# Kernel optimization log

Hardware: AMD Instinct MI355X
Metric: run time of the kernel (lower is better)

## Reference

```python
import jax, jax.numpy as jnp
import numpy as np

NUM_SLOTS = 16
CORE_INPUT_SIZE = 256


def _perm_matrix(key):
    p = jax.random.permutation(key, NUM_SLOTS)
    return jnp.eye(NUM_SLOTS, dtype=jnp.float32)[p]


def setup_inputs() -> dict:
    key = jax.random.key(0)
    kx, k1, k2 = jax.random.split(key, 3)
    x = jax.random.normal(kx, (512, 16, 16, CORE_INPUT_SIZE), dtype=jnp.float32)
    Ppos = _perm_matrix(k1)
    Pneg = _perm_matrix(k2)
    return {"x": x, "Ppos": Ppos, "Pneg": Pneg}


def reference(x, Ppos, Pneg):
    B, O, I, C = x.shape
    # split last dim into (num_slots rows, cols)
    xr = x.reshape(B, O, I, NUM_SLOTS, C // NUM_SLOTS)
    # permutation-matrix einsum on the slots axis (a one-hot gather)
    xpos = jnp.einsum('ij,boijk->boiik'.replace('boij', 'bOIj').replace('boii', 'bOIi'), Ppos, xr) if False else jnp.einsum('ij,...jk->...ik', Ppos, xr)
    xneg = jnp.einsum('ij,...jk->...ik', Pneg, xr)
    return (xpos - xneg).reshape(B, O, I, C)
```

## Files before the change

kernel.cpp:

```cpp
#include <hip/hip_runtime.h>


#define NSLOTS 16

__global__ __launch_bounds__(256) void permute_ws_kernel(
    const float4* __restrict__ x,
    const float* __restrict__ Ppos,
    const float* __restrict__ Pneg,
    float4* __restrict__ out,
    long total_v4)
{
    __shared__ int spos[NSLOTS];
    __shared__ int sneg[NSLOTS];

    const int t = threadIdx.x;
    if (t < NSLOTS) {
        int ip = 0, in_ = 0;
        #pragma unroll
        for (int j = 0; j < NSLOTS; ++j) {
            if (Ppos[t * NSLOTS + j] > 0.5f) ip = j;
            if (Pneg[t * NSLOTS + j] > 0.5f) in_ = j;
        }
        spos[t] = ip;
        sneg[t] = in_;
    }
    __syncthreads();

    long idx = (long)blockIdx.x * blockDim.x + threadIdx.x;
    const long stride = (long)gridDim.x * blockDim.x;

    for (; idx < total_v4; idx += stride) {
        const long row_base = idx & ~63L;
        const int  v        = (int)(idx & 63);
        const int  slot     = v >> 2;
        const int  k4       = v & 3;

        const float4 a = x[row_base + ((long)spos[slot] << 2) + k4];
        const float4 b = x[row_base + ((long)sneg[slot] << 2) + k4];

        float4 r;
        r.x = a.x - b.x;
        r.y = a.y - b.y;
        r.z = a.z - b.z;
        r.w = a.w - b.w;
        out[idx] = r;
    }
}

extern "C" void kernel_launch(void* const* d_in, const int* in_sizes, int n_in,
                              void* d_out, int out_size, void* d_ws, size_t ws_size,
                              hipStream_t stream)
{
    const float4* x    = (const float4*)d_in[0];
    const float*  Ppos = (const float*)d_in[1];
    const float*  Pneg = (const float*)d_in[2];
    float4*       out  = (float4*)d_out;

    const long total_v4 = (long)out_size / 4;

    const int block = 256;
    long blocks_needed = (total_v4 + block - 1) / block;
    int grid = (int)(blocks_needed > 32768 ? 32768 : blocks_needed);

    permute_ws_kernel<<<grid, block, 0, stream>>>(x, Ppos, Pneg, out, total_v4);
}
```

Measured before the change: 224.5 us.

## Replace gathered loads with one coalesced load and wavefront shuffles

Each thread now loads its own float4 contiguously, and the permuted source values are fetched from other lanes with __shfl, replacing two gathered global loads per output. Decoding of the permutation matrices moves into a separate tiny kernel that writes indices to workspace, which removes the per-block shared-memory decode and barrier. The change relies on each 64-lane wavefront covering exactly one 256-float row and on the grid stride staying a multiple of 64. It adds eight cross-lane shuffles per element and a second kernel launch.

Result: no change. 228.6 us (+1.9%).

```diff
diff --git a/kernel.cpp b/kernel.cpp
--- a/kernel.cpp
+++ b/kernel.cpp
@@ -3,42 +3,51 @@
 
 #define NSLOTS 16
 
+__global__ void decode_perm_kernel(const float* __restrict__ Ppos,
+                                   const float* __restrict__ Pneg,
+                                   int* __restrict__ wsi)
+{
+    const int t = threadIdx.x;
+    if (t < 2 * NSLOTS) {
+        const float* P = (t < NSLOTS) ? Ppos : Pneg;
+        const int row = t & (NSLOTS - 1);
+        int idx = 0;
+        #pragma unroll
+        for (int j = 0; j < NSLOTS; ++j)
+            if (P[row * NSLOTS + j] > 0.5f) idx = j;
+        wsi[t] = idx;
+    }
+}
+
 __global__ __launch_bounds__(256) void permute_ws_kernel(
     const float4* __restrict__ x,
-    const float* __restrict__ Ppos,
-    const float* __restrict__ Pneg,
+    const int* __restrict__ wsi,
     float4* __restrict__ out,
     long total_v4)
 {
-    __shared__ int spos[NSLOTS];
-    __shared__ int sneg[NSLOTS];
+    const int lane = threadIdx.x & 63;
+    const int slot = lane >> 2;
+    const int k4   = lane & 3;
 
-    const int t = threadIdx.x;
-    if (t < NSLOTS) {
-        int ip = 0, in_ = 0;
-        #pragma unroll
-        for (int j = 0; j < NSLOTS; ++j) {
-            if (Ppos[t * NSLOTS + j] > 0.5f) ip = j;
-            if (Pneg[t * NSLOTS + j] > 0.5f) in_ = j;
-        }
-        spos[t] = ip;
-        sneg[t] = in_;
-    }
-    __syncthreads();
+    const int src_a = (wsi[slot] << 2) | k4;
+    const int src_b = (wsi[NSLOTS + slot] << 2) | k4;
 
     long idx = (long)blockIdx.x * blockDim.x + threadIdx.x;
     const long stride = (long)gridDim.x * blockDim.x;
 
     for (; idx < total_v4; idx += stride) {
-        const long row_base = idx & ~63L;
-        const int  v        = (int)(idx & 63);
-        const int  slot     = v >> 2;
-        const int  k4       = v & 3;
+        const float4 v = x[idx];
 
-        const float4 a = x[row_base + ((long)spos[slot] << 2) + k4];
-        const float4 b = x[row_base + ((long)sneg[slot] << 2) + k4];
+        float4 a, b, r;
+        a.x = __shfl(v.x, src_a, 64);
+        a.y = __shfl(v.y, src_a, 64);
+        a.z = __shfl(v.z, src_a, 64);
+        a.w = __shfl(v.w, src_a, 64);
+        b.x = __shfl(v.x, src_b, 64);
+        b.y = __shfl(v.y, src_b, 64);
+        b.z = __shfl(v.z, src_b, 64);
+        b.w = __shfl(v.w, src_b, 64);
 
-        float4 r;
         r.x = a.x - b.x;
         r.y = a.y - b.y;
         r.z = a.z - b.z;
@@ -55,12 +64,14 @@
     const float*  Ppos = (const float*)d_in[1];
     const float*  Pneg = (const float*)d_in[2];
     float4*       out  = (float4*)d_out;
+    int*          wsi  = (int*)d_ws;
 
     const long total_v4 = (long)out_size / 4;
+
+    decode_perm_kernel<<<1, 64, 0, stream>>>(Ppos, Pneg, wsi);
 
     const int block = 256;
     long blocks_needed = (total_v4 + block - 1) / block;
     int grid = (int)(blocks_needed > 32768 ? 32768 : blocks_needed);
-
-    permute_ws_kernel<<<grid, block, 0, stream>>>(x, Ppos, Pneg, out, total_v4);
+    permute_ws_kernel<<<grid, block, 0, stream>>>(x, wsi, out, total_v4);
 }
```

## Load each row once and permute slots with wavefront shuffles

Applied to the files above, without the earlier changes.

Each thread now loads its own float4 in a coalesced way and gets the permuted values from other lanes with __shfl, instead of doing two gather loads per output. Every thread decodes the permutation indices itself, which removes the shared memory and the barrier. The grid is fixed at 2048 blocks and each iteration handles two elements to keep more loads in flight. The cost is 16 cross-lane shuffles per pair of elements. The code also assumes total_v4 is a multiple of 64 and that a wavefront holds exactly one 64-float4 row.

New measurement: 236.3 us. 1.05x slower.

```diff
diff --git a/kernel.cpp b/kernel.cpp
--- a/kernel.cpp
+++ b/kernel.cpp
@@ -10,40 +10,41 @@
     float4* __restrict__ out,
     long total_v4)
 {
-    __shared__ int spos[NSLOTS];
-    __shared__ int sneg[NSLOTS];
+    const int lane = threadIdx.x & 63;
+    const int slot = lane >> 2;
+    const int k4   = lane & 3;
 
-    const int t = threadIdx.x;
-    if (t < NSLOTS) {
-        int ip = 0, in_ = 0;
-        #pragma unroll
-        for (int j = 0; j < NSLOTS; ++j) {
-            if (Ppos[t * NSLOTS + j] > 0.5f) ip = j;
-            if (Pneg[t * NSLOTS + j] > 0.5f) in_ = j;
-        }
-        spos[t] = ip;
-        sneg[t] = in_;
+    int ip = 0, in_ = 0;
+    #pragma unroll
+    for (int j = 0; j < NSLOTS; ++j) {
+        if (Ppos[slot * NSLOTS + j] > 0.5f) ip = j;
+        if (Pneg[slot * NSLOTS + j] > 0.5f) in_ = j;
     }
-    __syncthreads();
+    const int src_a = (ip << 2) | k4;
+    const int src_b = (in_ << 2) | k4;
 
-    long idx = (long)blockIdx.x * blockDim.x + threadIdx.x;
+    long i = (long)blockIdx.x * blockDim.x + threadIdx.x;
     const long stride = (long)gridDim.x * blockDim.x;
 
-    for (; idx < total_v4; idx += stride) {
-        const long row_base = idx & ~63L;
-        const int  v        = (int)(idx & 63);
-        const int  slot     = v >> 2;
-        const int  k4       = v & 3;
+    for (; i < total_v4; i += 2 * stride) {
+        const long i1 = i + stride;
+        const bool has1 = (i1 < total_v4);
 
-        const float4 a = x[row_base + ((long)spos[slot] << 2) + k4];
-        const float4 b = x[row_base + ((long)sneg[slot] << 2) + k4];
+        const float4 v0 = x[i];
+        const float4 v1 = has1 ? x[i1] : v0;
 
-        float4 r;
-        r.x = a.x - b.x;
-        r.y = a.y - b.y;
-        r.z = a.z - b.z;
-        r.w = a.w - b.w;
-        out[idx] = r;
+        float4 r0, r1;
+        r0.x = __shfl(v0.x, src_a, 64) - __shfl(v0.x, src_b, 64);
+        r0.y = __shfl(v0.y, src_a, 64) - __shfl(v0.y, src_b, 64);
+        r0.z = __shfl(v0.z, src_a, 64) - __shfl(v0.z, src_b, 64);
+        r0.w = __shfl(v0.w, src_a, 64) - __shfl(v0.w, src_b, 64);
+        r1.x = __shfl(v1.x, src_a, 64) - __shfl(v1.x, src_b, 64);
+        r1.y = __shfl(v1.y, src_a, 64) - __shfl(v1.y, src_b, 64);
+        r1.z = __shfl(v1.z, src_a, 64) - __shfl(v1.z, src_b, 64);
+        r1.w = __shfl(v1.w, src_a, 64) - __shfl(v1.w, src_b, 64);
+
+        out[i] = r0;
+        if (has1) out[i1] = r1;
     }
 }
 
@@ -59,8 +60,6 @@
     const long total_v4 = (long)out_size / 4;
 
     const int block = 256;
-    long blocks_needed = (total_v4 + block - 1) / block;
-    int grid = (int)(blocks_needed > 32768 ? 32768 : blocks_needed);
-
+    const int grid  = 2048;
     permute_ws_kernel<<<grid, block, 0, stream>>>(x, Ppos, Pneg, out, total_v4);
 }
```
